# Optimization experiments

Hardware: AMD Instinct MI355X
Metric: run time of the kernel (lower is better)

The kernel has to match this reference:

```python
import jax, jax.numpy as jnp
import numpy as np
import math

N = 5000; K = 30; E = N * K
C_S, C_Z, C_A = 256, 128, 16
H, DH, P, L = 4, 64, 8, 4
NUM_AA = 21
NUM_RBF = 16; D_MIN, D_MAX = 2.0, 22.0
EPS = 1e-8

def _ln(x):
    mu = jnp.mean(x, -1, keepdims=True)
    var = jnp.mean((x - mu) ** 2, -1, keepdims=True)
    return (x - mu) * jax.lax.rsqrt(var + 1e-5)

def _inv_apply(rot, trans, x):
    # rigid invert_apply: R^T (x - t); rot [n,3,3], trans [n,3], x [n,p,3]
    return jnp.einsum('nji,npj->npi', rot, x - trans[:, None, :])

def _rbf(d):
    mu = jnp.linspace(D_MIN, D_MAX, NUM_RBF)
    sigma = (D_MAX - D_MIN) / NUM_RBF
    return jnp.exp(-(((d[..., None] - mu) / sigma) ** 2))

def _dihedral_feats(bb):
    X = bb.reshape(-1, 3)  # [3N,3] N,CA,C chain
    dX = X[1:] - X[:-1]
    U = dX / (jnp.linalg.norm(dX, axis=-1, keepdims=True) + EPS)
    u2, u1, u0 = U[:-2], U[1:-1], U[2:]
    n2 = jnp.cross(u2, u1); n2 = n2 / (jnp.linalg.norm(n2, axis=-1, keepdims=True) + EPS)
    n1 = jnp.cross(u1, u0); n1 = n1 / (jnp.linalg.norm(n1, axis=-1, keepdims=True) + EPS)
    cosD = jnp.clip(jnp.sum(n2 * n1, -1), -1 + 1e-7, 1 - 1e-7)
    D = jnp.sign(jnp.sum(u2 * n1, -1)) * jnp.arccos(cosD)
    D = jnp.pad(D, (1, 2)).reshape(-1, 3)  # [N,3]
    return jnp.concatenate([jnp.cos(D), jnp.sin(D)], -1)  # [N,6]

def _virtual_cb(n, ca, c):
    b = ca - n; cc = c - ca; a = jnp.cross(b, cc)
    return -0.58273431 * a + 0.56802827 * b - 0.54067466 * cc + ca

def _prep(seq, atom14, rot, trans, res_mask, mgm_mask, noising_mask, atom14_exists, edge_index, atom_tab):
    res_f = res_mask.astype(jnp.float32)
    mgm_f = mgm_mask.astype(jnp.float32)
    bb = atom14[:, :3]
    dih = _dihedral_feats(bb)
    seq_oh = jax.nn.one_hot(seq, NUM_AA)
    node_vec = _inv_apply(rot, trans, atom14[:, :4])  # [N,4,3]
    node_raw = jnp.concatenate([dih, mgm_f[:, None], seq_oh * mgm_f[:, None], node_vec.reshape(N, -1)], -1) * res_f[:, None]
    sc = jnp.where(jnp.arange(14) >= 4, mgm_f[:, None], 1.0)  # zero hidden side-chain atoms
    am_f = jnp.where(jnp.arange(14) >= 4, mgm_mask[:, None], atom14_exists).astype(jnp.float32)
    atom_raw = atom_tab[seq] * sc[..., None]  # [N,14,9]
    dsti, srci = edge_index[0], edge_index[1]
    nsrc = noising_mask[srci].astype(jnp.float32); ndst = noising_mask[dsti].astype(jnp.float32)
    cb = _virtual_cb(bb[:, 0], bb[:, 1], bb[:, 2])
    bb4 = jnp.concatenate([bb, cb[:, None]], 1)  # [N,4,3]
    dist = jnp.linalg.norm(bb4[srci][:, :, None] - bb4[dsti][:, None, :] + EPS, axis=-1)  # [E,4,4]
    rbf = _rbf(dist).reshape(E, -1)  # [E,256]
    dpos = (dsti - srci).astype(jnp.float32)
    freq = jnp.exp(jnp.arange(0, 16, 2, dtype=jnp.float32) * (-math.log(10000.0) / 16))
    ang = dpos[:, None] * freq
    pe = jnp.concatenate([jnp.cos(ang), jnp.sin(ang)], -1)  # [E,16]
    bb_local = _inv_apply(rot, trans, bb4)
    src_local = bb_local[srci].reshape(E, -1) * (1 - nsrc)[:, None]
    dst_in_src = jnp.einsum('eji,epj->epi', rot[srci], bb4[dsti] - trans[srci][:, None, :]).reshape(E, -1) * (1 - ndst)[:, None]
    edge_mask = res_mask[srci] & res_mask[dsti]
    edge_raw = jnp.concatenate([ndst[:, None], nsrc[:, None], seq_oh[srci] * (1 - nsrc)[:, None], seq_oh[dsti] * (1 - ndst)[:, None], rbf, pe, src_local, dst_in_src], -1) * edge_mask.astype(jnp.float32)[:, None]
    return node_raw, edge_raw, atom_raw, res_f, am_f, edge_mask

def _mlp3(x, W1, W2, W3):
    return _ln(jax.nn.relu(jax.nn.relu(x @ W1) @ W2) @ W3)

def _net(node_raw, edge_raw, atom_raw, res_f, am_f, edge_mask, rot, trans, edge_index, Wn1, Wn2, Wn3, Wez1, Wez2, Wez3, Wa1, Wa2, Wa3, Wq, Wk, Wv, Wqp, Wkp, Wb, gamma, Wo, Wau, Wt1, Wt2, Wne, We1, We2, Wp1, Wp2, Wmu, Wlv):
    s = _mlp3(node_raw, Wn1, Wn2, Wn3)    # [N,256]
    z = _mlp3(edge_raw, Wez1, Wez2, Wez3) # [E,128]
    af = _mlp3(atom_raw, Wa1, Wa2, Wa3)   # [N,14,16]
    dsti, srci = edge_index[0], edge_index[1]
    em_f = edge_mask.astype(jnp.float32)
    w_pt = math.sqrt(2.0 / (9 * P)); w_l = math.sqrt(1.0 / 3.0)
    for l in range(L):
        q = (s @ Wq[l]).reshape(N, H, DH); k = (s @ Wk[l]).reshape(N, H, DH); v = (s @ Wv[l]).reshape(N, H, DH)
        qp = (s @ Wqp[l]).reshape(N, H, P, 3); kp = (s @ Wkp[l]).reshape(N, H, P, 3)
        qg = jnp.einsum('nij,nhpj->nhpi', rot, qp) + trans[:, None, None, :]
        kg = jnp.einsum('nij,nhpj->nhpi', rot, kp) + trans[:, None, None, :]
        logits = (jnp.sum(q[dsti] * k[srci], -1) * (w_l / math.sqrt(DH))
                  + w_l * (z @ Wb[l])
                  - 0.5 * w_pt * jax.nn.softplus(gamma[l]) * jnp.sum((qg[dsti] - kg[srci]) ** 2, (-2, -1)))
        logits = jnp.where(edge_mask[:, None], logits, -1e9)
        m = jax.ops.segment_max(logits, dsti, num_segments=N)
        a = jnp.exp(logits - m[dsti]) * em_f[:, None]
        a = a / (jax.ops.segment_sum(a, dsti, num_segments=N) + 1e-9)[dsti]
        ov = jax.ops.segment_sum(a[..., None] * v[srci], dsti, num_segments=N).reshape(N, -1)
        og = jax.ops.segment_sum(a[..., None, None] * kg[srci], dsti, num_segments=N)
        ol = jnp.einsum('nji,nhpj->nhpi', rot, og - trans[:, None, None, :])
        on = jnp.sqrt(jnp.sum(ol ** 2, -1) + EPS)
        s = _ln(s + jnp.concatenate([ov, ol.reshape(N, -1), on.reshape(N, -1)], -1) @ Wo[l])
        af = _ln(af + jnp.concatenate([af, jnp.broadcast_to(s[:, None, :], (N, 14, C_S))], -1) @ Wau[l])
        s = _ln(s + jax.nn.relu(s @ Wt1[l]) @ Wt2[l]) * res_f[:, None]
        h = s @ Wne[l]
        z = _ln(jax.nn.relu(jnp.concatenate([z, h[dsti], h[srci]], -1) @ We1[l]) @ We2[l]) * em_f[:, None]
        af = _ln(af + jax.nn.relu(af @ Wp1[l]) @ Wp2[l]) * am_f[..., None]
    return jnp.concatenate([s @ Wmu, s @ Wlv], -1)  # [N,512] = [mu | logvar]

def setup_inputs():
    ks = jax.random.split(jax.random.key(0), 40)
    w = lambda i, shp: jax.random.normal(ks[i], shp, dtype=jnp.float32) * 0.02
    return {
        'seq': jax.random.randint(ks[0], (N,), 0, NUM_AA, dtype=jnp.int32),
        'atom14': jax.random.normal(ks[1], (N, 14, 3), dtype=jnp.float32) * 3.0,
        'rot': jax.random.normal(ks[2], (N, 3, 3), dtype=jnp.float32),
        'trans': jax.random.normal(ks[3], (N, 3), dtype=jnp.float32) * 3.0,
        'res_mask': jnp.ones((N,), dtype=bool),
        'mgm_mask': jax.random.bernoulli(ks[4], 0.5, (N,)),
        'noising_mask': jax.random.bernoulli(ks[5], 0.5, (N,)),
        'atom14_exists': jnp.ones((N, 14), dtype=bool),
        'edge_index': jax.random.randint(ks[6], (2, E), 0, N, dtype=jnp.int32),
        'atom_tab': jax.random.uniform(ks[7], (NUM_AA + 1, 14, 9), dtype=jnp.float32),
        'Wn1': w(8, (40, 512)), 'Wn2': w(9, (512, 512)), 'Wn3': w(10, (512, 256)),
        'Wez1': w(11, (340, 256)), 'Wez2': w(12, (256, 256)), 'Wez3': w(13, (256, 128)),
        'Wa1': w(14, (9, 32)), 'Wa2': w(15, (32, 32)), 'Wa3': w(16, (32, 16)),
        'Wq': w(17, (L, 256, 256)), 'Wk': w(18, (L, 256, 256)), 'Wv': w(19, (L, 256, 256)),
        'Wqp': w(20, (L, 256, H * P * 3)), 'Wkp': w(21, (L, 256, H * P * 3)),
        'Wb': w(22, (L, 128, H)), 'gamma': w(23, (L, H)),
        'Wo': w(24, (L, H * (DH + 4 * P), 256)), 'Wau': w(25, (L, C_A + C_S, C_A)),
        'Wt1': w(26, (L, 256, 256)), 'Wt2': w(27, (L, 256, 256)),
        'Wne': w(28, (L, 256, 128)), 'We1': w(29, (L, 384, 256)), 'We2': w(30, (L, 256, 128)),
        'Wp1': w(31, (L, 16, 16)), 'Wp2': w(32, (L, 16, 16)),
        'Wmu': w(33, (256, 256)), 'Wlv': w(34, (256, 256)),
    }

def reference(seq, atom14, rot, trans, res_mask, mgm_mask, noising_mask, atom14_exists, edge_index, atom_tab, Wn1, Wn2, Wn3, Wez1, Wez2, Wez3, Wa1, Wa2, Wa3, Wq, Wk, Wv, Wqp, Wkp, Wb, gamma, Wo, Wau, Wt1, Wt2, Wne, We1, We2, Wp1, Wp2, Wmu, Wlv):
    prep = _prep(seq, atom14, rot, trans, res_mask, mgm_mask, noising_mask, atom14_exists, edge_index, atom_tab)
    return _net(*prep, rot, trans, edge_index, Wn1, Wn2, Wn3, Wez1, Wez2, Wez3, Wa1, Wa2, Wa3, Wq, Wk, Wv, Wqp, Wkp, Wb, gamma, Wo, Wau, Wt1, Wt2, Wne, We1, We2, Wp1, Wp2, Wmu, Wlv)
```

## Files before the change

### kernel.cpp

```cpp
#include <hip/hip_runtime.h>
#include <hip/hip_bf16.h>

#define NR 5000
#define EE 150000
#define NA14 (NR*14)
#define EPSF 1e-8f

typedef unsigned short ushort;
typedef __attribute__((ext_vector_type(8))) short bf16x8;
typedef __attribute__((ext_vector_type(4))) float f32x4;

#define GLDS16(gp, lp) __builtin_amdgcn_global_load_lds( \
    (__attribute__((address_space(1))) void*)(gp), \
    (__attribute__((address_space(3))) void*)(lp), 16, 0, 0)

static __device__ __forceinline__ float wsum64(float v) {
#pragma unroll
  for (int o = 1; o < 64; o <<= 1) v += __shfl_xor(v, o, 64);
  return v;
}
static __device__ __forceinline__ ushort f2b(float f) {
  union { float f; unsigned u; } x; x.f = f;
  unsigned r = (x.u + 0x7FFF + ((x.u >> 16) & 1)) >> 16;
  return (ushort)r;
// ... 305 lines not shown
  const int wm = (w >> 1) * 64;
  const int wn = (w & 1) * 64;
  const int bm = blockIdx.x * 128;
  const int bn = blockIdx.y * 128;
  const int rl0 = tid >> 2;
  const int sl  = tid & 3;
  const int rl1 = rl0 + 64;
  const int ks0 = (sl - rl0 - (rl0 >> 2)) & 3;
  const int ks1 = (sl - rl1 - (rl1 >> 2)) & 3;
  int ar0 = bm + rl0; if (ar0 >= M) ar0 = M - 1;
  int ar1 = bm + rl1; if (ar1 >= M) ar1 = M - 1;
  const ushort* gA0 = A + (size_t)ar0 * lda + ks0 * 8;
  const ushort* gA1 = A + (size_t)ar1 * lda + ks1 * 8;
  const ushort* gB0 = BT + (size_t)(bn + rl0) * Kd + ks0 * 8;
  const ushort* gB1 = BT + (size_t)(bn + rl1) * Kd + ks1 * 8;

  auto stage = [&](int buf, int k0) {
    GLDS16(gA0 + k0, &As[buf][rl0][sl][0]);
    GLDS16(gB0 + k0, &Bs[buf][rl0][sl][0]);
    GLDS16(gA1 + k0, &As[buf][rl1][sl][0]);
    GLDS16(gB1 + k0, &Bs[buf][rl1][sl][0]);
  };

  f32x4 zero4 = {0.f, 0.f, 0.f, 0.f};
  f32x4 acc[4][4];
#pragma unroll
  for (int i = 0; i < 4; ++i)
#pragma unroll
    for (int j = 0; j < 4; ++j) acc[i][j] = zero4;

  stage(0, 0);
  asm volatile("s_waitcnt vmcnt(0)" ::: "memory");
  __builtin_amdgcn_s_barrier();

  const int nt = Kd >> 5;
  for (int t = 0; t < nt; ++t) {
    int cur = t & 1;
    if (t + 1 < nt) stage(cur ^ 1, (t + 1) << 5);
    {
      const int ksr = lane >> 4, lr = lane & 15;
      bf16x8 af[4], bf[4];
#pragma unroll
      for (int i = 0; i < 4; ++i) {
        int row = wm + i*16 + lr;
        int sa = (ksr + row + (row >> 2)) & 3;
        af[i] = *reinterpret_cast<const bf16x8*>(&As[cur][row][sa][0]);
      }
#pragma unroll
      for (int j = 0; j < 4; ++j) {
        int col = wn + j*16 + lr;
        int sb = (ksr + col + (col >> 2)) & 3;
        bf[j] = *reinterpret_cast<const bf16x8*>(&Bs[cur][col][sb][0]);
      }
#pragma unroll
      for (int i = 0; i < 4; ++i)
#pragma unroll
        for (int j = 0; j < 4; ++j)
          acc[i][j] = __builtin_amdgcn_mfma_f32_16x16x32_bf16(af[i], bf[j], acc[i][j], 0, 0, 0);
    }
    asm volatile("s_waitcnt vmcnt(0) lgkmcnt(0)" ::: "memory");
    __builtin_amdgcn_s_barrier();
  }

  int lr = lane & 15, lg = lane >> 4;
  if (LNZ) {
    float* stats = (float*)As;
#pragma unroll
    for (int i = 0; i < 4; ++i) {
#pragma unroll
      for (int rg = 0; rg < 4; ++rg) {
        float ps = 0.f, pq = 0.f;
#pragma unroll
        for (int j = 0; j < 4; ++j) {
          float v = b2f(f2b(acc[i][j][rg]));
          ps += v; pq += v * v;
        }
#pragma unroll
        for (int o = 1; o < 16; o <<= 1) {
          ps += __shfl_xor(ps, o, 64);
          pq += __shfl_xor(pq, o, 64);
        }
        if (lr == 0) {
          int row = wm + i*16 + lg*4 + rg;
          stats[(row * 2 + (wn >> 6)) * 2 + 0] = ps;
          stats[(row * 2 + (wn >> 6)) * 2 + 1] = pq;
        }
      }
    }
    __syncthreads();
#pragma unroll
    for (int i = 0; i < 4; ++i) {
#pragma unroll
      for (int rg = 0; rg < 4; ++rg) {
        int row = wm + i*16 + lg*4 + rg;
        int m = bm + row;
        float s0 = stats[(row*2 + 0)*2 + 0] + stats[(row*2 + 1)*2 + 0];
        float q0 = stats[(row*2 + 0)*2 + 1] + stats[(row*2 + 1)*2 + 1];
        float mu = s0 * (1.f / 128.f);
        float var = q0 * (1.f / 128.f) - mu * mu;
        float rs = rsqrtf(var + 1e-5f);
        if (m < M) {
          float sc = lnsc ? lnsc[m] : 1.f;
#pragma unroll
          for (int j = 0; j < 4; ++j) {
            int cc = wn + j*16 + lr;
            float v = b2f(f2b(acc[i][j][rg]));
            Cb[(size_t)m * 128 + cc] = f2b((v - mu) * rs * sc);
          }
        }
      }
    }
  } else if (PERMOUT) {
    const int pc = bn + wn + lr * 4;
#pragma unroll
    for (int i = 0; i < 4; ++i) {
#pragma unroll
      for (int rg = 0; rg < 4; ++rg) {
        int m = bm + wm + i*16 + lg*4 + rg;
        if (m >= M) continue;
        float v0 = acc[i][0][rg], v1 = acc[i][1][rg];
        float v2 = acc[i][2][rg], v3 = acc[i][3][rg];
        if (EPADD) {
          int de = dsti[m], se = srci[m];
          uint2 hd = *reinterpret_cast<const uint2*>(HD + (size_t)de * Ncols + pc);
          uint2 hs = *reinterpret_cast<const uint2*>(HS + (size_t)se * Ncols + pc);
          v0 += blo(hd.x) + blo(hs.x);
          v1 += bhi(hd.x) + bhi(hs.x);
          v2 += blo(hd.y) + blo(hs.y);
          v3 += bhi(hd.y) + bhi(hs.y);
        }
        if (RELU) {
          v0 = fmaxf(v0, 0.f); v1 = fmaxf(v1, 0.f);
          v2 = fmaxf(v2, 0.f); v3 = fmaxf(v3, 0.f);
        }
        uint2 p;
        p.x = (unsigned)f2b(v0) | ((unsigned)f2b(v1) << 16);
        p.y = (unsigned)f2b(v2) | ((unsigned)f2b(v3) << 16);
        *reinterpret_cast<uint2*>(Cb + (size_t)m * Ncols + pc) = p;
      }
    }
  } else {
#pragma unroll
    for (int i = 0; i < 4; ++i) {
#pragma unroll
      for (int rg = 0; rg < 4; ++rg) {
        int m = bm + wm + i*16 + lg*4 + rg;
        if (m >= M) continue;
#pragma unroll
        for (int j = 0; j < 4; ++j) {
          int cc = bn + wn + j*16 + lr;
          float v = acc[i][j][rg];
          if (RELU) v = fmaxf(v, 0.f);
          if (OUTBF) Cb[(size_t)m * Ncols + cc] = f2b(v);
          else       Cf[(size_t)m * Ncols + cc] = v;
        }
      }
    }
  }
}

__global__ void k_gemm(const float* __restrict__ A, const float* __restrict__ B,
                       float* __restrict__ C, int M, int Ncols, int Kd,
                       int ldc, int coff, int relu) {
  __shared__ float As[16][68];
  __shared__ float Bs[16][64];
  const int tid = threadIdx.x;
  const int bm = blockIdx.x * 64;
  const int bn = blockIdx.y * 64;
  const int tm = tid >> 4;
  const int tn = tid & 15;
  const int arow = tid >> 2;
  const int akq = (tid & 3) << 2;
  const int brow = tid >> 4;
  const int bcol = (tid & 15) << 2;
  float acc[4][4] = {{0.f}};
  const int am = bm + arow;
  for (int k0 = 0; k0 < Kd; k0 += 16) {
    float av[4];
#pragma unroll
    for (int j = 0; j < 4; ++j) {
      int k = k0 + akq + j;
      av[j] = (am < M && k < Kd) ? A[(size_t)am * Kd + k] : 0.f;
    }
#pragma unroll
    for (int j = 0; j < 4; ++j) As[akq + j][arow] = av[j];
    int kb = k0 + brow;
    float bv[4];
    if (kb < Kd) {
#pragma unroll
      for (int j = 0; j < 4; ++j) {
        int c = bn + bcol + j;
        bv[j] = (c < Ncols) ? B[(size_t)kb * Ncols + c] : 0.f;
      }
    } else { bv[0]=bv[1]=bv[2]=bv[3]=0.f; }
    *reinterpret_cast<float4*>(&Bs[brow][bcol]) = make_float4(bv[0],bv[1],bv[2],bv[3]);
    __syncthreads();
#pragma unroll
    for (int kk = 0; kk < 16; ++kk) {
      float4 a4 = *reinterpret_cast<const float4*>(&As[kk][tm << 2]);
      float4 b4 = *reinterpret_cast<const float4*>(&Bs[kk][tn << 2]);
      float aa[4] = {a4.x, a4.y, a4.z, a4.w};
      float bb[4] = {b4.x, b4.y, b4.z, b4.w};
#pragma unroll
      for (int i = 0; i < 4; ++i)
#pragma unroll
        for (int j = 0; j < 4; ++j)
          acc[i][j] = fmaf(aa[i], bb[j], acc[i][j]);
    }
    __syncthreads();
  }
#pragma unroll
  for (int i = 0; i < 4; ++i) {
    int m = bm + (tm << 2) + i;
    if (m >= M) continue;
#pragma unroll
    for (int j = 0; j < 4; ++j) {
      int c = bn + (tn << 2) + j;
      if (c >= Ncols) continue;
      float v = acc[i][j];
      if (relu) v = fmaxf(v, 0.f);
      C[(size_t)m * ldc + coff + c] = v;
    }
  }
}

__global__ void k_small_gemm(const float* __restrict__ A, const float* __restrict__ B,
                             float* __restrict__ C, int M, int Ncols, int Kd, int relu) {
  __shared__ float Ws[1024];
  int t = threadIdx.x;
  int nw = Kd * Ncols;
  for (int i = t; i < nw; i += 256) Ws[i] = B[i];
  __syncthreads();
  int rpb = 256 / Ncols;
  int r = blockIdx.x * rpb + t / Ncols;
  int c = t - (t / Ncols) * Ncols;
  if (r >= M || t >= rpb * Ncols) return;
  const float* a = A + (size_t)r * Kd;
  float s = 0.f;
  for (int k = 0; k < Kd; ++k) s = fmaf(a[k], Ws[k * Ncols + c], s);
  if (relu) s = fmaxf(s, 0.f);
  C[(size_t)r * Ncols + c] = s;
}

__global__ void k_ln(float* __restrict__ dst, ushort* __restrict__ dstb,
                     const float* __restrict__ res, const float* __restrict__ x,
                     const float* __restrict__ rowscale, int M) {
  int r = blockIdx.x * 4 + (threadIdx.x >> 6);
  if (r >= M) return;
  int l = threadIdx.x & 63;
  size_t base = (size_t)r * 256 + l * 4;
  float4 v = *reinterpret_cast<const float4*>(x + base);
  if (res) {
    float4 rv = *reinterpret_cast<const float4*>(res + base);
    v.x += rv.x; v.y += rv.y; v.z += rv.z; v.w += rv.w;
  }
  float s = wsum64(v.x + v.y + v.z + v.w);
  float mu = s * (1.f / 256.f);
  float d0 = v.x-mu, d1 = v.y-mu, d2 = v.z-mu, d3 = v.w-mu;
  float s2 = wsum64(d0*d0 + d1*d1 + d2*d2 + d3*d3);
  float rs = rsqrtf(s2 * (1.f / 256.f) + 1e-5f);
  float sc = rowscale ? rowscale[r] : 1.f;
  float o0 = d0*rs*sc, o1 = d1*rs*sc, o2 = d2*rs*sc, o3 = d3*rs*sc;
  *reinterpret_cast<float4*>(dst + base) = make_float4(o0, o1, o2, o3);
  if (dstb) {
    uint2 p;
    p.x = (unsigned)f2b(o0) | ((unsigned)f2b(o1) << 16);
    p.y = (unsigned)f2b(o2) | ((unsigned)f2b(o3) << 16);
    *reinterpret_cast<uint2*>(dstb + base) = p;
  }
}

__global__ void k_ln16(float* __restrict__ af, int M) {
  int r = blockIdx.x * 256 + threadIdx.x;
  if (r >= M) return;
  float x[16]; float s = 0.f;
#pragma unroll
  for (int j = 0; j < 16; ++j) { x[j] = af[(size_t)r*16 + j]; s += x[j]; }
  float mu = s * (1.f/16.f);
  float v = 0.f;
#pragma unroll
  for (int j = 0; j < 16; ++j) { float d = x[j]-mu; v += d*d; }
  float rs = rsqrtf(v * (1.f/16.f) + 1e-5f);
#pragma unroll
  for (int j = 0; j < 16; ++j) af[(size_t)r*16 + j] = (x[j]-mu)*rs;
}


__global__ void k_qg(const float* __restrict__ rot, const float* __restrict__ trans,
                     const float* __restrict__ pp,
                     float* __restrict__ qg, float* __restrict__ kg) {
  int idx = blockIdx.x * 256 + threadIdx.x;
  if (idx >= NR * 64) return;
  int n = idx >> 6; int w = (idx >> 5) & 1; int hp = idx & 31;
  const float* src = pp + (size_t)n*256 + (w ? 96 : 0) + hp*3;
  float* dstp = (w ? kg : qg) + (size_t)n*96 + hp*3;
  const float* R = rot + (size_t)n*9;
  const float* t = trans + (size_t)n*3;
  float s0 = src[0], s1 = src[1], s2 = src[2];
#pragma unroll
  for (int i = 0; i < 3; ++i)
    dstp[i] = R[i*3+0]*s0 + R[i*3+1]*s1 + R[i*3+2]*s2 + t[i];
}

__global__ void k_logits(const int* __restrict__ dsti, const int* __restrict__ srci,
                         const float* __restrict__ emf, const ushort* __restrict__ qkv,
                         const ushort* __restrict__ z,
                         const float* __restrict__ qg, const float* __restrict__ kg,
                         const float* __restrict__ WbT, const float* __restrict__ coef,
                         float* __restrict__ logits) {
  int e = blockIdx.x * 4 + (threadIdx.x >> 6);
  int l = threadIdx.x & 63;
  int hh = l >> 4, t = l & 15;
  int d = dsti[e], s = srci[e];
  const float wl = 0.57735026918962576f;
  const float qk_scale = wl * 0.125f;
  uint2 qw = *reinterpret_cast<const uint2*>(qkv + (size_t)d*768 + hh*64 + t*4);
  uint2 kw = *reinterpret_cast<const uint2*>(qkv + (size_t)s*768 + 256 + hh*64 + t*4);
  float acc = qk_scale * (blo(qw.x)*blo(kw.x) + bhi(qw.x)*bhi(kw.x)
                        + blo(qw.y)*blo(kw.y) + bhi(qw.y)*bhi(kw.y));
  {
    uint4 zw = *reinterpret_cast<const uint4*>(z + (size_t)e*128 + t*8);
    const float* wb = WbT + hh*128 + t*8;
    float4 w0 = *reinterpret_cast<const float4*>(wb);
    float4 w1 = *reinterpret_cast<const float4*>(wb + 4);
    float zsum = blo(zw.x)*w0.x + bhi(zw.x)*w0.y + blo(zw.y)*w0.z + bhi(zw.y)*w0.w
               + blo(zw.z)*w1.x + bhi(zw.z)*w1.y + blo(zw.w)*w1.z + bhi(zw.w)*w1.w;
    acc += wl * zsum;
  }
  {
    float cf = coef[hh];
    int c = hh*24 + t;
    float dq = qg[(size_t)d*96 + c] - kg[(size_t)s*96 + c];
    acc -= cf * dq * dq;
    if (t < 8) {
      int c2 = c + 16;
      float dq2 = qg[(size_t)d*96 + c2] - kg[(size_t)s*96 + c2];
      acc -= cf * dq2 * dq2;
    }
  }
#pragma unroll
  for (int o = 1; o < 16; o <<= 1) acc += __shfl_xor(acc, o, 64);
  if (t == 0) {
    float em = emf[e];
    logits[(size_t)e*4 + hh] = (em > 0.f) ? acc : -1e9f;
  }
}

__global__ void k_attn(const int* __restrict__ offs, const int* __restrict__ eord,
                       const int* __restrict__ srci, const float* __restrict__ logits,
                       const float* __restrict__ emf, const ushort* __restrict__ qkv,
                       const float* __restrict__ kg, ushort* __restrict__ catb,
                       float* __restrict__ og) {
  int n = blockIdx.x; int l = threadIdx.x;
  int e0 = offs[n], e1 = offs[n+1];
  float m[4] = {-1e30f,-1e30f,-1e30f,-1e30f};
  for (int i = e0; i < e1; ++i) {
    int e = eord[i];
#pragma unroll
    for (int h = 0; h < 4; ++h) m[h] = fmaxf(m[h], logits[(size_t)e*4 + h]);
  }
  float den[4] = {0.f,0.f,0.f,0.f};
  float accv[4] = {0.f,0.f,0.f,0.f};
  float acg0 = 0.f, acg1 = 0.f;
  int hg0 = l / 24;
  int hg1 = (64 + l) / 24;
  for (int i = e0; i < e1; ++i) {
    int e = eord[i]; int s = srci[e];
    float em = emf[e];
    float a[4];
#pragma unroll
    for (int h = 0; h < 4; ++h) {
      a[h] = expf(logits[(size_t)e*4 + h] - m[h]) * em;
      den[h] += a[h];
    }
#pragma unroll
    for (int j = 0; j < 4; ++j)
      accv[j] = fmaf(a[j], b2f(qkv[(size_t)s*768 + 512 + j*64 + l]), accv[j]);
    acg0 = fmaf(a[hg0], kg[(size_t)s*96 + l], acg0);
    if (l < 32) acg1 = fmaf(a[hg1], kg[(size_t)s*96 + 64 + l], acg1);
  }
#pragma unroll
  for (int j = 0; j < 4; ++j)
    catb[(size_t)n*384 + j*64 + l] = f2b(accv[j] / (den[j] + 1e-9f));
  og[(size_t)n*96 + l] = acg0 / (den[hg0] + 1e-9f);
  if (l < 32) og[(size_t)n*96 + 64 + l] = acg1 / (den[hg1] + 1e-9f);
}

__global__ void k_olon(const float* __restrict__ rot, const float* __restrict__ trans,
                       const float* __restrict__ og, ushort* __restrict__ catb) {
  int idx = blockIdx.x * 256 + threadIdx.x;
  if (idx >= NR * 32) return;
  int n = idx >> 5, hp = idx & 31;
  const float* R = rot + (size_t)n*9;
  const float* t = trans + (size_t)n*3;
  const float* o = og + (size_t)n*96 + hp*3;
  float d0 = o[0]-t[0], d1 = o[1]-t[1], d2 = o[2]-t[2];
  float ol[3];
#pragma unroll
  for (int i = 0; i < 3; ++i)
    ol[i] = R[0*3+i]*d0 + R[1*3+i]*d1 + R[2*3+i]*d2;
  ushort* cp = catb + (size_t)n*384;
  cp[256 + hp*3 + 0] = f2b(ol[0]);
  cp[256 + hp*3 + 1] = f2b(ol[1]);
  cp[256 + hp*3 + 2] = f2b(ol[2]);
  cp[352 + hp] = f2b(sqrtf(ol[0]*ol[0] + ol[1]*ol[1] + ol[2]*ol[2] + EPSF));
}

__global__ void k_af_wau(float* __restrict__ af, const float* __restrict__ WauA,
                         const float* __restrict__ t1) {
  __shared__ float W[256];
  int t = threadIdx.x;
  W[t] = WauA[t];
  __syncthreads();
  int r = blockIdx.x * 256 + t;
  if (r >= NA14) return;
  int n = r / 14;
  float x[16], y[16];
#pragma unroll
  for (int j = 0; j < 16; ++j) x[j] = af[(size_t)r*16 + j];
#pragma unroll
  for (int j = 0; j < 16; ++j) y[j] = t1[(size_t)n*16 + j];
#pragma unroll
  for (int k = 0; k < 16; ++k) {
    float xv = x[k];
#pragma unroll
    for (int j = 0; j < 16; ++j) y[j] = fmaf(xv, W[k*16 + j], y[j]);
  }
  float v[16]; float s = 0.f;
#pragma unroll
  for (int j = 0; j < 16; ++j) { v[j] = x[j] + y[j]; s += v[j]; }
  float mu = s * (1.f/16.f);
  float var = 0.f;
#pragma unroll
  for (int j = 0; j < 16; ++j) { float d = v[j]-mu; var += d*d; }
  float rs = rsqrtf(var * (1.f/16.f) + 1e-5f);
#pragma unroll
  for (int j = 0; j < 16; ++j) af[(size_t)r*16 + j] = (v[j]-mu)*rs;
}

__global__ void k_af_p(float* __restrict__ af, const float* __restrict__ Wp1,
                       const float* __restrict__ Wp2, const float* __restrict__ amf) {
  __shared__ float W1[256], W2[256];
  int t = threadIdx.x;
  W1[t] = Wp1[t]; W2[t] = Wp2[t];
  __syncthreads();
  int r = blockIdx.x * 256 + t;
  if (r >= NA14) return;
  float x[16];
#pragma unroll
  for (int j = 0; j < 16; ++j) x[j] = af[(size_t)r*16 + j];
  float h1[16];
#pragma unroll
  for (int j = 0; j < 16; ++j) h1[j] = 0.f;
#pragma unroll
  for (int k = 0; k < 16; ++k) {
    float xv = x[k];
#pragma unroll
    for (int j = 0; j < 16; ++j) h1[j] = fmaf(xv, W1[k*16 + j], h1[j]);
  }
#pragma unroll
  for (int j = 0; j < 16; ++j) h1[j] = fmaxf(h1[j], 0.f);
  float h2[16];
#pragma unroll
  for (int j = 0; j < 16; ++j) h2[j] = 0.f;
#pragma unroll
  for (int k = 0; k < 16; ++k) {
    float xv = h1[k];
#pragma unroll
    for (int j = 0; j < 16; ++j) h2[j] = fmaf(xv, W2[k*16 + j], h2[j]);
  }
  float v[16]; float s = 0.f;
#pragma unroll
  for (int j = 0; j < 16; ++j) { v[j] = x[j] + h2[j]; s += v[j]; }
  float mu = s * (1.f/16.f);
  float var = 0.f;
#pragma unroll
  for (int j = 0; j < 16; ++j) { float d = v[j]-mu; var += d*d; }
  float rs = rsqrtf(var * (1.f/16.f) + 1e-5f);
  float am = amf[r];
#pragma unroll
  for (int j = 0; j < 16; ++j) af[(size_t)r*16 + j] = (v[j]-mu)*rs*am;
}

__global__ void k_sentinel(float* __restrict__ out, float val) {
  if (threadIdx.x == 0 && blockIdx.x == 0) out[0] = val;
}


extern "C" void kernel_launch(void* const* d_in, const int* in_sizes, int n_in,
                              void* d_out, int out_size, void* d_ws, size_t ws_size,
                              hipStream_t stream) {
  (void)in_sizes; (void)n_in; (void)out_size;
  const int*   seq    = (const int*)  d_in[0];
  const float* atom14 = (const float*)d_in[1];
  const float* rot    = (const float*)d_in[2];
  const float* trans  = (const float*)d_in[3];
  const int*   rmask  = (const int*)  d_in[4];
  const int*   mgm    = (const int*)  d_in[5];
  const int*   nmask  = (const int*)  d_in[6];
  const int*   a14ex  = (const int*)  d_in[7];
  const int*   eidx   = (const int*)  d_in[8];
  const int*   dsti   = eidx;
  const int*   srci   = eidx + EE;
  const float* atab   = (const float*)d_in[9];
  const float* Wn1 = (const float*)d_in[10];
  const float* Wn2 = (const float*)d_in[11];
  const float* Wn3 = (const float*)d_in[12];
  const float* Wez1 = (const float*)d_in[13];
  const float* Wez2 = (const float*)d_in[14];
  const float* Wez3 = (const float*)d_in[15];
  const float* Wa1 = (const float*)d_in[16];
  const float* Wa2 = (const float*)d_in[17];
  const float* Wa3 = (const float*)d_in[18];
  const float* Wq  = (const float*)d_in[19];
  const float* Wk  = (const float*)d_in[20];
  const float* Wv  = (const float*)d_in[21];
  const float* Wqp = (const float*)d_in[22];
  const float* Wkp = (const float*)d_in[23];
  const float* Wb  = (const float*)d_in[24];
  const float* gam = (const float*)d_in[25];
  const float* Wo  = (const float*)d_in[26];
  const float* Wau = (const float*)d_in[27];
  const float* Wt1 = (const float*)d_in[28];
  const float* Wt2 = (const float*)d_in[29];
  const float* Wne = (const float*)d_in[30];
  const float* We1 = (const float*)d_in[31];
  const float* We2 = (const float*)d_in[32];
  const float* Wp1 = (const float*)d_in[33];
  const float* Wp2 = (const float*)d_in[34];
  const float* Wmu = (const float*)d_in[35];
  const float* Wlv = (const float*)d_in[36];
  float* out = (float*)d_out;

  float* ws = (float*)d_ws;
  size_t WSF = ws_size / sizeof(float);
  size_t off = 0;
  auto alloc = [&](size_t n) { n = (n + 3) & ~(size_t)3; float* p = ws + off; off += n; return p; };

  ushort* Zb  = (ushort*)alloc((size_t)EE * 64);
  float* S    = alloc((size_t)NR * 256);
  ushort* SB  = (ushort*)alloc((size_t)NR * 128);
  float* AF   = alloc((size_t)NA14 * 16);
  float* AMF  = alloc(NA14);
  float* EMF  = alloc(EE);
  float* LOG  = alloc((size_t)EE * 4);
  float* RESF = alloc(NR);
  float* DP   = alloc(3 * NR);
  float* BB4  = alloc((size_t)NR * 12);
  float* BBL  = alloc((size_t)NR * 12);
  ushort* NRAWB = (ushort*)alloc((size_t)NR * 32);
  float* ARAW = alloc((size_t)NA14 * 9);
  ushort* WezT1 = (ushort*)alloc(45056);
  ushort* WezT2 = (ushort*)alloc(32768);
  ushort* WezT3 = (ushort*)alloc(16384);
  ushort* We1zT = (ushort*)alloc(65536);
  ushort* We1dT = (ushort*)alloc(65536);
  ushort* We1sT = (ushort*)alloc(65536);
  ushort* We2T  = (ushort*)alloc(65536);
  ushort* WqkvT = (ushort*)alloc(393216);
  ushort* WppT  = (ushort*)alloc(131072);
  ushort* WoT   = (ushort*)alloc(196608);
  ushort* Wt1T  = (ushort*)alloc(131072);
  ushort* Wt2T  = (ushort*)alloc(131072);
  ushort* WneT  = (ushort*)alloc(65536);
  ushort* WmuLvT= (ushort*)alloc(65536);
  ushort* Wn1T  = (ushort*)alloc(16384);
  ushort* Wn2T  = (ushort*)alloc(131072);
  ushort* Wn3T  = (ushort*)alloc(65536);
  float* WBT  = alloc(2048);
  float* COEF = alloc(16);
  ushort* QKVB= (ushort*)alloc((size_t)NR * 384);
  float* PP   = alloc((size_t)NR * 256);
  float* QG   = alloc((size_t)NR * 96);
  float* KG   = alloc((size_t)NR * 96);
  ushort* CATB= (ushort*)alloc((size_t)NR * 192);
  float* OGb  = alloc((size_t)NR * 96);
  float* NBUF = alloc((size_t)NR * 256);
  ushort* HbB = (ushort*)alloc((size_t)NR * 64);
  ushort* HDb = (ushort*)alloc((size_t)NR * 128);
  ushort* HSb = (ushort*)alloc((size_t)NR * 128);
  float* T1   = alloc((size_t)NR * 16);
  ushort* NB1b = (ushort*)alloc((size_t)NR * 256);
  ushort* NB2b = (ushort*)alloc((size_t)NR * 256);
  ushort* TRHb = (ushort*)alloc((size_t)NR * 128);
  float* AH1  = alloc((size_t)NA14 * 32);
  float* AH2  = alloc((size_t)NA14 * 32);
  int* CNT  = (int*)alloc(NR);
  int* OFFS = (int*)alloc(NR + 1);
  int* EORD = (int*)alloc(EE);
  size_t fixedF = off;

  if (fixedF + (size_t)432 * 1024 > WSF) {
    k_sentinel<<<1, 64, 0, stream>>>(out, 1.0e6f * (float)(ws_size >> 20));
    return;
  }
  float* EAR = ws + fixedF;
  size_t arenaF = WSF - fixedF;
  int CH_P = (int)((arenaF / 432 > (size_t)EE) ? (size_t)EE : arenaF / 432);
  int CH_L = (int)((arenaF / 128 > (size_t)EE) ? (size_t)EE : arenaF / 128);
  ushort* ERb = (ushort*)EAR;
  ushort* B1b = ERb + (size_t)CH_P * 352;
  ushort* B2b = B1b + (size_t)CH_P * 256;
  ushort* EARb = (ushort*)EAR;

  auto wT = [&](const float* W, ushort* WTp, int K, int N, int Kpad,
                long ss, long ds, int L, int perm) {
    long tot = (long)N * Kpad * L;
    k_wT<<<(int)((tot + 255) / 256), 256, 0, stream>>>(W, WTp, K, N, Kpad, ss, ds, L, perm);
  };

  wT(Wez1, WezT1, 340, 256, 352, 0, 0, 1, 0);
  wT(Wez2, WezT2, 256, 256, 256, 0, 0, 1, 1);
  wT(Wez3, WezT3, 256, 128, 256, 0, 0, 1, 1);
  wT(Wn1, Wn1T, 40, 512, 64, 0, 0, 1, 0);
  wT(Wn2, Wn2T, 512, 512, 512, 0, 0, 1, 1);
  wT(Wn3, Wn3T, 512, 256, 512, 0, 0, 1, 1);
  wT(We1,         We1zT, 128, 256, 128, 98304, 32768, 4, 0);
  wT(We1 + 32768, We1dT, 128, 256, 128, 98304, 32768, 4, 0);
  wT(We1 + 65536, We1sT, 128, 256, 128, 98304, 32768, 4, 0);
  wT(We2, We2T, 256, 128, 256, 32768, 32768, 4, 1);
  wT(Wo,  WoT,  384, 256, 384, 98304, 98304, 4, 0);
  wT(Wt1, Wt1T, 256, 256, 256, 65536, 65536, 4, 0);
  wT(Wt2, Wt2T, 256, 256, 256, 65536, 65536, 4, 1);
  wT(Wne, WneT, 256, 128, 256, 32768, 32768, 4, 0);
  wT(Wmu, WmuLvT, 256, 256, 256, 0, 0, 1, 0);
  wT(Wlv, WmuLvT + 65536, 256, 256, 256, 0, 0, 1, 0);
  wT(Wq,  WqkvT + 0,       256, 256, 256, 65536, 196608, 4, 0);
  wT(Wk,  WqkvT + 65536,   256, 256, 256, 65536, 196608, 4, 0);
  wT(Wv,  WqkvT + 131072,  256, 256, 256, 65536, 196608, 4, 0);
  wT(Wqp, WppT + 0,        256,  96, 256, 24576, 65536, 4, 0);
  wT(Wkp, WppT + 24576,    256,  96, 256, 24576, 65536, 4, 0);
  k_zero_us<<<(64*256*4 + 255)/256, 256, 0, stream>>>(WppT + 49152, 64*256, 65536, 4);
  k_wbT<<<8, 256, 0, stream>>>(Wb, WBT);
  k_coef<<<1, 64, 0, stream>>>(gam, COEF);

  k_masks<<<(NR + 255) / 256, 256, 0, stream>>>(rmask, RESF);
  k_dihedral<<<(3 * NR + 255) / 256, 256, 0, stream>>>(atom14, DP);
  k_bb4<<<(NR + 255) / 256, 256, 0, stream>>>(atom14, rot, trans, BB4, BBL);
  k_noderaw<<<NR, 64, 0, stream>>>(seq, atom14, rot, trans, DP, rmask, mgm, NRAWB);
  k_atomraw<<<(NA14 + 255) / 256, 256, 0, stream>>>(seq, mgm, a14ex, atab, ARAW, AMF);

  {
    dim3 g1((NR + 127) / 128, 4), g2((NR + 127) / 128, 4), g3((NR + 127) / 128, 2);
    k_mgemm<1,1,0,1,0><<<g1, 256, 0, stream>>>(NRAWB, Wn1T, nullptr, NB1b, NR, 512, 64, 64,
                                               nullptr, nullptr, nullptr, nullptr, nullptr);
    k_mgemm<1,1,0,1,0><<<g2, 256, 0, stream>>>(NB1b, Wn2T, nullptr, NB2b, NR, 512, 512, 512,
                                               nullptr, nullptr, nullptr, nullptr, nullptr);
    k_mgemm<0,0,0,0,0><<<g3, 256, 0, stream>>>(NB2b, Wn3T, NBUF, nullptr, NR, 256, 512, 512,
                                               nullptr, nullptr, nullptr, nullptr, nullptr);
  }
  k_ln<<<(NR + 3) / 4, 256, 0, stream>>>(S, SB, nullptr, NBUF, nullptr, NR);

  k_small_gemm<<<(NA14 + 7) / 8, 256, 0, stream>>>(ARAW, Wa1, AH1, NA14, 32, 9, 1);
  k_small_gemm<<<(NA14 + 7) / 8, 256, 0, stream>>>(AH1, Wa2, AH2, NA14, 32, 32, 1);
  k_small_gemm<<<(NA14 + 15) / 16, 256, 0, stream>>>(AH2, Wa3, AF, NA14, 16, 32, 0);
  k_ln16<<<(NA14 + 255) / 256, 256, 0, stream>>>(AF, NA14);

  k_zero_int<<<(NR + 255) / 256, 256, 0, stream>>>(CNT, NR);
  k_count<<<(EE + 255) / 256, 256, 0, stream>>>(dsti, CNT);
  k_scan<<<1, 256, 0, stream>>>(CNT, OFFS);
  k_zero_int<<<(NR + 255) / 256, 256, 0, stream>>>(CNT, NR);
  k_place<<<(EE + 255) / 256, 256, 0, stream>>>(dsti, OFFS, CNT, EORD);
  k_sortwave<<<NR, 64, 0, stream>>>(OFFS, EORD);

  for (int e0 = 0; e0 < EE; e0 += CH_P) {
    int cnt = (EE - e0 < CH_P) ? (EE - e0) : CH_P;
    k_edgeraw<<<(cnt + 3) / 4, 256, 0, stream>>>(dsti, srci, seq, rmask, nmask,
                                                 BB4, BBL, rot, trans, ERb, EMF, e0, cnt);
    dim3 g1((cnt + 127) / 128, 2), g2((cnt + 127) / 128, 2), g3((cnt + 127) / 128, 1);
    k_mgemm<1,1,0,1,0><<<g1, 256, 0, stream>>>(ERb, WezT1, nullptr, B1b, cnt, 256, 352, 352,
                                               nullptr, nullptr, nullptr, nullptr, nullptr);
    k_mgemm<1,1,0,1,0><<<g2, 256, 0, stream>>>(B1b, WezT2, nullptr, B2b, cnt, 256, 256, 256,
                                               nullptr, nullptr, nullptr, nullptr, nullptr);
    k_mgemm<0,1,0,0,1><<<g3, 256, 0, stream>>>(B2b, WezT3, nullptr, Zb + (size_t)e0 * 128,
                                               cnt, 128, 256, 256,
                                               nullptr, nullptr, nullptr, nullptr, nullptr);
  }

  for (int l = 0; l < 4; ++l) {
    const ushort* WqkvT_l = WqkvT + (size_t)l * 196608;
    const ushort* WppT_l  = WppT  + (size_t)l * 65536;
    const ushort* WoT_l = WoT + (size_t)l * 98304;
    const float* Wau_l = Wau + (size_t)l * 4352;
    const ushort* Wt1T_l = Wt1T + (size_t)l * 65536;
    const ushort* Wt2T_l = Wt2T + (size_t)l * 65536;
    const ushort* WneT_l = WneT + (size_t)l * 32768;
    const ushort* We1zT_l = We1zT + (size_t)l * 32768;
    const ushort* We1dT_l = We1dT + (size_t)l * 32768;
    const ushort* We1sT_l = We1sT + (size_t)l * 32768;
    const ushort* We2T_l = We2T + (size_t)l * 32768;
    const float* Wp1_l = Wp1 + (size_t)l * 256;
    const float* Wp2_l = Wp2 + (size_t)l * 256;

    {
      dim3 gq((NR + 127) / 128, 6);
      k_mgemm<0,1,0,0,0><<<gq, 256, 0, stream>>>(SB, WqkvT_l, nullptr, QKVB, NR, 768, 256, 256,
                                                 nullptr, nullptr, nullptr, nullptr, nullptr);
      dim3 gp((NR + 127) / 128, 2);
      k_mgemm<0,0,0,0,0><<<gp, 256, 0, stream>>>(SB, WppT_l, PP, nullptr, NR, 256, 256, 256,
                                                 nullptr, nullptr, nullptr, nullptr, nullptr);
    }
    k_qg<<<(NR * 64 + 255) / 256, 256, 0, stream>>>(rot, trans, PP, QG, KG);
    k_logits<<<EE / 4, 256, 0, stream>>>(dsti, srci, EMF, QKVB, Zb, QG, KG,
                                         WBT + (size_t)l * 512, COEF + (size_t)l * 4, LOG);
    k_attn<<<NR, 64, 0, stream>>>(OFFS, EORD, srci, LOG, EMF, QKVB, KG, CATB, OGb);
    k_olon<<<(NR * 32 + 255) / 256, 256, 0, stream>>>(rot, trans, OGb, CATB);
    {
      dim3 g((NR + 127) / 128, 2);
      k_mgemm<0,0,0,0,0><<<g, 256, 0, stream>>>(CATB, WoT_l, NBUF, nullptr, NR, 256, 384, 384,
                                                nullptr, nullptr, nullptr, nullptr, nullptr);
    }
    k_ln<<<(NR + 3) / 4, 256, 0, stream>>>(S, SB, S, NBUF, nullptr, NR);
    {
      dim3 g((NR + 63) / 64, 1);
      k_gemm<<<g, 256, 0, stream>>>(S, Wau_l + 256, T1, NR, 16, 256, 16, 0, 0);
    }
    k_af_wau<<<(NA14 + 255) / 256, 256, 0, stream>>>(AF, Wau_l, T1);
    {
      dim3 g((NR + 127) / 128, 2);
      k_mgemm<1,1,0,1,0><<<g, 256, 0, stream>>>(SB, Wt1T_l, nullptr, TRHb, NR, 256, 256, 256,
                                                nullptr, nullptr, nullptr, nullptr, nullptr);
      k_mgemm<0,0,0,0,0><<<g, 256, 0, stream>>>(TRHb, Wt2T_l, NBUF, nullptr, NR, 256, 256, 256,
                                                nullptr, nullptr, nullptr, nullptr, nullptr);
    }
    k_ln<<<(NR + 3) / 4, 256, 0, stream>>>(S, SB, S, NBUF, RESF, NR);
    {
      dim3 g((NR + 127) / 128, 1);
      k_mgemm<0,1,0,0,0><<<g, 256, 0, stream>>>(SB, WneT_l, nullptr, HbB, NR, 128, 256, 256,
                                                nullptr, nullptr, nullptr, nullptr, nullptr);
    }
    {
      dim3 g((NR + 127) / 128, 2);
      k_mgemm<0,1,0,1,0><<<g, 256, 0, stream>>>(HbB, We1dT_l, nullptr, HDb, NR, 256, 128, 128,
                                                nullptr, nullptr, nullptr, nullptr, nullptr);
      k_mgemm<0,1,0,1,0><<<g, 256, 0, stream>>>(HbB, We1sT_l, nullptr, HSb, NR, 256, 128, 128,
                                                nullptr, nullptr, nullptr, nullptr, nullptr);
    }
    for (int e0 = 0; e0 < EE; e0 += CH_L) {
      int cnt = (EE - e0 < CH_L) ? (EE - e0) : CH_L;
      dim3 g1((cnt + 127) / 128, 2), g2((cnt + 127) / 128, 1);
      k_mgemm<1,1,1,1,0><<<g1, 256, 0, stream>>>(Zb + (size_t)e0 * 128, We1zT_l, nullptr, EARb,
                                                 cnt, 256, 128, 128,
                                                 HDb, HSb, dsti + e0, srci + e0, nullptr);
      k_mgemm<0,1,0,0,1><<<g2, 256, 0, stream>>>(EARb, We2T_l, nullptr, Zb + (size_t)e0 * 128,
                                                 cnt, 128, 256, 256,
                                                 nullptr, nullptr, nullptr, nullptr, EMF + e0);
    }
    k_af_p<<<(NA14 + 255) / 256, 256, 0, stream>>>(AF, Wp1_l, Wp2_l, AMF);
  }

  {
    dim3 g((NR + 127) / 128, 4);
    k_mgemm<0,0,0,0,0><<<g, 256, 0, stream>>>(SB, WmuLvT, out, nullptr, NR, 512, 256, 256,
                                              nullptr, nullptr, nullptr, nullptr, nullptr);
  }
}
```

Measured before the change: 1.899 ms.

## Fuse attention logits into aggregation kernel with online softmax

After: 1.845 ms. -2.8%, faster.

```diff
diff --git a/kernel.cpp b/kernel.cpp
--- a/kernel.cpp
+++ b/kernel.cpp
@@ -631,82 +631,69 @@
     dstp[i] = R[i*3+0]*s0 + R[i*3+1]*s1 + R[i*3+2]*s2 + t[i];
 }
 
-__global__ void k_logits(const int* __restrict__ dsti, const int* __restrict__ srci,
-                         const float* __restrict__ emf, const ushort* __restrict__ qkv,
-                         const ushort* __restrict__ z,
-                         const float* __restrict__ qg, const float* __restrict__ kg,
-                         const float* __restrict__ WbT, const float* __restrict__ coef,
-                         float* __restrict__ logits) {
-  int e = blockIdx.x * 4 + (threadIdx.x >> 6);
-  int l = threadIdx.x & 63;
+__global__ void k_attn2(const int* __restrict__ offs, const int* __restrict__ eord,
+                        const int* __restrict__ srci, const float* __restrict__ emf,
+                        const ushort* __restrict__ qkv, const ushort* __restrict__ z,
+                        const float* __restrict__ qg, const float* __restrict__ kg,
+                        const float* __restrict__ WbT, const float* __restrict__ coef,
+                        ushort* __restrict__ catb, float* __restrict__ og) {
+  int n = blockIdx.x; int l = threadIdx.x;
   int hh = l >> 4, t = l & 15;
-  int d = dsti[e], s = srci[e];
+  int e0 = offs[n], e1 = offs[n+1];
   const float wl = 0.57735026918962576f;
   const float qk_scale = wl * 0.125f;
-  uint2 qw = *reinterpret_cast<const uint2*>(qkv + (size_t)d*768 + hh*64 + t*4);
-  uint2 kw = *reinterpret_cast<const uint2*>(qkv + (size_t)s*768 + 256 + hh*64 + t*4);
-  float acc = qk_scale * (blo(qw.x)*blo(kw.x) + bhi(qw.x)*bhi(kw.x)
-                        + blo(qw.y)*blo(kw.y) + bhi(qw.y)*bhi(kw.y));
-  {
-    uint4 zw = *reinterpret_cast<const uint4*>(z + (size_t)e*128 + t*8);
-    const float* wb = WbT + hh*128 + t*8;
-    float4 w0 = *reinterpret_cast<const float4*>(wb);
-    float4 w1 = *reinterpret_cast<const float4*>(wb + 4);
-    float zsum = blo(zw.x)*w0.x + bhi(zw.x)*w0.y + blo(zw.y)*w0.z + bhi(zw.y)*w0.w
-               + blo(zw.z)*w1.x + bhi(zw.z)*w1.y + blo(zw.w)*w1.z + bhi(zw.w)*w1.w;
-    acc += wl * zsum;
-  }
-  {
-    float cf = coef[hh];
-    int c = hh*24 + t;
-    float dq = qg[(size_t)d*96 + c] - kg[(size_t)s*96 + c];
-    acc -= cf * dq * dq;
-    if (t < 8) {
-      int c2 = c + 16;
-      float dq2 = qg[(size_t)d*96 + c2] - kg[(size_t)s*96 + c2];
-      acc -= cf * dq2 * dq2;
-    }
-  }
-#pragma unroll
-  for (int o = 1; o < 16; o <<= 1) acc += __shfl_xor(acc, o, 64);
-  if (t == 0) {
-    float em = emf[e];
-    logits[(size_t)e*4 + hh] = (em > 0.f) ? acc : -1e9f;
-  }
-}
-
-__global__ void k_attn(const int* __restrict__ offs, const int* __restrict__ eord,
-                       const int* __restrict__ srci, const float* __restrict__ logits,
-                       const float* __restrict__ emf, const ushort* __restrict__ qkv,
-                       const float* __restrict__ kg, ushort* __restrict__ catb,
-                       float* __restrict__ og) {
-  int n = blockIdx.x; int l = threadIdx.x;
-  int e0 = offs[n], e1 = offs[n+1];
+  uint2 qw = *reinterpret_cast<const uint2*>(qkv + (size_t)n*768 + hh*64 + t*4);
+  float q0 = blo(qw.x), q1 = bhi(qw.x), q2 = blo(qw.y), q3 = bhi(qw.y);
+  float qg1 = qg[(size_t)n*96 + hh*24 + t];
+  float qg2 = (t < 8) ? qg[(size_t)n*96 + hh*24 + t + 16] : 0.f;
+  float cf = coef[hh];
+  int hg0 = l / 24;
+  int hg1 = (64 + l) / 24;
+
   float m[4] = {-1e30f,-1e30f,-1e30f,-1e30f};
-  for (int i = e0; i < e1; ++i) {
-    int e = eord[i];
-#pragma unroll
-    for (int h = 0; h < 4; ++h) m[h] = fmaxf(m[h], logits[(size_t)e*4 + h]);
-  }
   float den[4] = {0.f,0.f,0.f,0.f};
   float accv[4] = {0.f,0.f,0.f,0.f};
   float acg0 = 0.f, acg1 = 0.f;
-  int hg0 = l / 24;
-  int hg1 = (64 + l) / 24;
+
   for (int i = e0; i < e1; ++i) {
     int e = eord[i]; int s = srci[e];
     float em = emf[e];
-    float a[4];
+    uint2 kw = *reinterpret_cast<const uint2*>(qkv + (size_t)s*768 + 256 + hh*64 + t*4);
+    float acc = qk_scale * (q0*blo(kw.x) + q1*bhi(kw.x) + q2*blo(kw.y) + q3*bhi(kw.y));
+    {
+      uint4 zw = *reinterpret_cast<const uint4*>(z + (size_t)e*128 + t*8);
+      const float* wb = WbT + hh*128 + t*8;
+      float4 w0 = *reinterpret_cast<const float4*>(wb);
+      float4 w1 = *reinterpret_cast<const float4*>(wb + 4);
+      acc += wl * (blo(zw.x)*w0.x + bhi(zw.x)*w0.y + blo(zw.y)*w0.z + bhi(zw.y)*w0.w
+                 + blo(zw.z)*w1.x + bhi(zw.z)*w1.y + blo(zw.w)*w1.z + bhi(zw.w)*w1.w);
+    }
+    {
+      float dq = qg1 - kg[(size_t)s*96 + hh*24 + t];
+      acc -= cf * dq * dq;
+      if (t < 8) {
+        float dq2 = qg2 - kg[(size_t)s*96 + hh*24 + t + 16];
+        acc -= cf * dq2 * dq2;
+      }
+    }
+#pragma unroll
+    for (int o = 1; o < 16; o <<= 1) acc += __shfl_xor(acc, o, 64);
+    float a[4], r[4];
 #pragma unroll
     for (int h = 0; h < 4; ++h) {
-      a[h] = expf(logits[(size_t)e*4 + h] - m[h]) * em;
-      den[h] += a[h];
+      float vh = __shfl(acc, h*16, 64);
+      float lg = (em > 0.f) ? vh : -1e9f;
+      float mn = m[h];
+      r[h] = 1.f;
+      if (lg > mn) { r[h] = expf(mn - lg); mn = lg; m[h] = mn; }
+      a[h] = expf(lg - mn) * em;
+      den[h] = den[h] * r[h] + a[h];
     }
 #pragma unroll
     for (int j = 0; j < 4; ++j)
-      accv[j] = fmaf(a[j], b2f(qkv[(size_t)s*768 + 512 + j*64 + l]), accv[j]);
-    acg0 = fmaf(a[hg0], kg[(size_t)s*96 + l], acg0);
-    if (l < 32) acg1 = fmaf(a[hg1], kg[(size_t)s*96 + 64 + l], acg1);
+      accv[j] = accv[j] * r[j] + a[j] * b2f(qkv[(size_t)s*768 + 512 + j*64 + l]);
+    acg0 = acg0 * r[hg0] + a[hg0] * kg[(size_t)s*96 + l];
+    if (l < 32) acg1 = acg1 * r[hg1] + a[hg1] * kg[(size_t)s*96 + 64 + l];
   }
 #pragma unroll
   for (int j = 0; j < 4; ++j)
@@ -931,6 +918,7 @@
   ushort* B1b = ERb + (size_t)CH_P * 352;
   ushort* B2b = B1b + (size_t)CH_P * 256;
   ushort* EARb = (ushort*)EAR;
+  (void)LOG;
 
   auto wT = [&](const float* W, ushort* WTp, int K, int N, int Kpad,
                 long ss, long ds, int L, int perm) {
@@ -1030,9 +1018,9 @@
                                                  nullptr, nullptr, nullptr, nullptr, nullptr);
     }
     k_qg<<<(NR * 64 + 255) / 256, 256, 0, stream>>>(rot, trans, PP, QG, KG);
-    k_logits<<<EE / 4, 256, 0, stream>>>(dsti, srci, EMF, QKVB, Zb, QG, KG,
-                                         WBT + (size_t)l * 512, COEF + (size_t)l * 4, LOG);
-    k_attn<<<NR, 64, 0, stream>>>(OFFS, EORD, srci, LOG, EMF, QKVB, KG, CATB, OGb);
+    k_attn2<<<NR, 64, 0, stream>>>(OFFS, EORD, srci, EMF, QKVB, Zb, QG, KG,
+                                   WBT + (size_t)l * 512, COEF + (size_t)l * 4,
+                                   CATB, OGb);
     k_olon<<<(NR * 32 + 255) / 256, 256, 0, stream>>>(rot, trans, OGb, CATB);
     {
       dim3 g((NR + 127) / 128, 2);
```
